# Kernel optimization log

Measured on AMD Instinct MI355X. Metric: run time of the kernel, lower is better.

## Reference

```python
import jax, jax.numpy as jnp
import numpy as np

BS, FH, FW, NA = 32, 100, 100, 9
IMG_H, IMG_W = 1600, 1600
STRIDE = 16
KEEP_PRE, KEEP_POST, NMS_THR = 1000, 300, 0.7


def _grid_anchors():
    scales = np.array([128.0, 256.0, 512.0])
    ratios = np.array([0.5, 1.0, 2.0])
    ws, hs = [], []
    for s in scales:
        for r in ratios:
            ws.append(s * np.sqrt(1.0 / r))
            hs.append(s * np.sqrt(r))
    ws, hs = np.array(ws), np.array(hs)  # [9]
    sx = (np.arange(FW) + 0.5) * STRIDE
    sy = (np.arange(FH) + 0.5) * STRIDE
    cx, cy = np.meshgrid(sx, sy)  # [FH,FW]
    cx = cx.reshape(-1, 1)
    cy = cy.reshape(-1, 1)
    anchors = np.stack([
        cx - 0.5 * ws, cy - 0.5 * hs, cx + 0.5 * ws, cy + 0.5 * hs
    ], axis=-1).reshape(-1, 4)  # [FH*FW*NA, 4]
    return anchors.astype(np.float32)


def setup_inputs() -> dict:
    key = jax.random.key(0)
    k1, k2 = jax.random.split(key)
    N = FH * FW * NA
    cls_logits = jax.random.normal(k1, (BS, N, 1), dtype=jnp.float32)
    reg_deltas = jax.random.normal(k2, (BS, N, 4), dtype=jnp.float32) * 0.3
    anchors = jnp.asarray(_grid_anchors())
    return {"cls_logits": cls_logits, "reg_deltas": reg_deltas,
            "anchors": anchors, "img_h": IMG_H, "img_w": IMG_W}


def _offsets2boxes(deltas, anchors):
    # deltas: [bs,N,4] (dx,dy,dw,dh); anchors: [N,4] xyxy
    aw = anchors[:, 2] - anchors[:, 0]
    ah = anchors[:, 3] - anchors[:, 1]
    acx = anchors[:, 0] + 0.5 * aw
    acy = anchors[:, 1] + 0.5 * ah
    cx = deltas[..., 0] * aw + acx
    cy = deltas[..., 1] * ah + acy
    w = jnp.exp(deltas[..., 2]) * aw
    h = jnp.exp(deltas[..., 3]) * ah
    return jnp.stack([cx - 0.5 * w, cy - 0.5 * h, cx + 0.5 * w, cy + 0.5 * h], axis=-1)


def _iou_matrix(b):
    # b: [K,4] -> [K,K]
    area = (b[:, 2] - b[:, 0]) * (b[:, 3] - b[:, 1])
    lt = jnp.maximum(b[:, None, :2], b[None, :, :2])
    rb = jnp.minimum(b[:, None, 2:], b[None, :, 2:])
    wh = jnp.clip(rb - lt, 0.0)
    inter = wh[..., 0] * wh[..., 1]
    return inter / (area[:, None] + area[None, :] - inter + 1e-12)


def _detect_single(boxes, scores, img_h, img_w):
    # boxes: [N,4], scores: [N]
    top_scores, idx = jax.lax.top_k(scores, KEEP_PRE)
    b = boxes[idx]  # [K,4], already score-sorted descending
    b = jnp.stack([
        jnp.clip(b[:, 0], 0.0, img_w), jnp.clip(b[:, 1], 0.0, img_h),
        jnp.clip(b[:, 2], 0.0, img_w), jnp.clip(b[:, 3], 0.0, img_h)
    ], axis=-1)
    iou = _iou_matrix(b)  # [K,K]
    K = KEEP_PRE
    cols = jnp.arange(K)

    def body(i, keep):
        # if box i still kept, suppress later boxes with IoU > thr (greedy NMS)
        sup = keep[i] & (iou[i] > NMS_THR) & (cols > i)
        return keep & ~sup

    keep = jax.lax.fori_loop(0, K, body, jnp.ones((K,), dtype=bool))
    # kept boxes first (stable sort preserves descending-score order), take top P
    order = jnp.argsort(~keep, stable=True)[:KEEP_POST]
    valid = keep[order]
    det = jnp.concatenate([b[order], top_scores[order, None]], axis=-1)
    return det * valid[:, None].astype(det.dtype)  # padded rows zeroed


def reference(cls_logits, reg_deltas, anchors, img_h, img_w):
    bs = cls_logits.shape[0]
    scores = jax.nn.sigmoid(cls_logits.reshape(bs, -1))  # [bs,N]
    boxes = _offsets2boxes(reg_deltas.reshape(bs, -1, 4), anchors)  # [bs,N,4]
    fh = jnp.float32(img_h)
    fw = jnp.float32(img_w)
    dets = jax.vmap(lambda b, s: _detect_single(b, s, fh, fw))(boxes, scores)
    return dets  # [bs, KEEP_POST, 5] (xmin,ymin,xmax,ymax,score), zero-padded
```

## Files before the change

### kernel.cpp

```cpp
#include <hip/hip_runtime.h>
#include <stdint.h>

#pragma clang fp contract(off)

#define BS 32
#define NANCH 90000
#define KEEP_PRE 1000
#define KEEP_POST 300
#define NMS_THR 0.7f
#define NBINS 4096
#define HREP 4129
#define CAND_MAX 4096
#define MW 16
#define NF4 22500

typedef unsigned long long u64;
typedef unsigned int u32;

#define BOX_OFF    0
#define SCORE_OFF  (BOX_OFF + (size_t)BS * KEEP_PRE * 16)
#define MASK_OFF   (SCORE_OFF + (size_t)BS * KEEP_PRE * 4)

__device__ __forceinline__ u32 fmono(float f) {
    u32 u = __float_as_uint(f);
    return (u & 0x80000000u) ? ~u : (u | 0x80000000u);
}

__global__ __launch_bounds__(1024) void prep_kernel(const float* __restrict__ logits,
                                                    const float* __restrict__ deltas,
                                                    const float* __restrict__ anchors,
                                                    float4* __restrict__ selbox,
                                                    float* __restrict__ selscore,
                                                    const int* __restrict__ p_img_h,
                                                    const int* __restrict__ p_img_w) {
    __shared__ u32 lh[2][HREP];
    __shared__ u32 S[NBINS + 1];
    __shared__ u64 grp[CAND_MAX];
    __shared__ u32 wtot[16], wexc[16];
    __shared__ u32 s_B;
    const int b = blockIdx.x;
    const int tid = threadIdx.x;
    const u32 lane = tid & 63;
    const int wv = tid >> 6;
    u32* h0 = lh[0];
    u32* h1 = lh[1];

    for (int i = tid; i < 2 * HREP; i += 1024) ((u32*)lh)[i] = 0;
    __syncthreads();

    const float4* src4 = (const float4*)(logits + (size_t)b * NANCH);
    u32* myh = lh[tid & 1];

#define H1_(f) do { u32 m_ = fmono(f); atomicAdd(&myh[m_ >> 20], 1u); } while (0)
#define HIST4_(v) do { H1_((v).x); H1_((v).y); H1_((v).z); H1_((v).w); } while (0)

    for (int j = 0; j < 20; j += 4) {
        float4 va = src4[tid + (j + 0) * 1024];
        float4 vb = src4[tid + (j + 1) * 1024];
        float4 vc = src4[tid + (j + 2) * 1024];
        float4 vd = src4[tid + (j + 3) * 1024];
        HIST4_(va); HIST4_(vb); HIST4_(vc); HIST4_(vd);
    }
    {
        float4 ve = src4[tid + 20 * 1024];
        HIST4_(ve);
        if (tid < NF4 - 21 * 1024) {
            float4 vf = src4[tid + 21 * 1024];
            HIST4_(vf);
        }
    }
    __syncthreads();

    const int g = tid * 4;
    const u32 c0 = h0[g] + h1[g];
    const u32 c1 = h0[g + 1] + h1[g + 1];
    const u32 c2 = h0[g + 2] + h1[g + 2];
    const u32 c3 = h0[g + 3] + h1[g + 3];
    {
        u32 s = c0 + c1 + c2 + c3;
#pragma unroll
        for (int off = 1; off < 64; off <<= 1) {
            u32 x = __shfl_down(s, off);
            if (lane + off < 64) s += x;
        }
        if (lane == 0) wtot[wv] = s;
        __syncthreads();
        if (tid < 16) {
            u32 v = wtot[tid];
            u32 t = v;
#pragma unroll
            for (int off = 1; off < 16; off <<= 1) {
                u32 x = __shfl_down(t, off);
                if (tid + off < 16) t += x;
            }
            wexc[tid] = t - v;
        }
        __syncthreads();
        const u32 base = wexc[wv] + s;
        S[g]     = base;
        S[g + 1] = base - c0;
        S[g + 2] = base - c0 - c1;
        S[g + 3] = base - c0 - c1 - c2;
        if (tid == 1023) S[NBINS] = 0;
    }
    __syncthreads();

    {
#pragma unroll
        for (int k = 0; k < 4; k++) {
            int bin = g + k;
            if (S[bin] >= KEEP_PRE && S[bin + 1] < KEEP_PRE) s_B = (u32)bin;
        }
        h0[g] = 0; h0[g + 1] = 0; h0[g + 2] = 0; h0[g + 3] = 0;
    }
    __syncthreads();
    const u32 B = s_B;
    const int n_cap = (int)min(S[B], (u32)CAND_MAX);
    u32* fill = h0;

    for (int j = 0; j < 22; ++j) {
        int idx4 = tid + (j << 10);
        if (idx4 >= NF4) break;
        float4 v = src4[idx4];
        u32 mm[4];
        mm[0] = fmono(v.x); mm[1] = fmono(v.y); mm[2] = fmono(v.z); mm[3] = fmono(v.w);
#pragma unroll
        for (int k = 0; k < 4; k++) {
            u32 bin = mm[k] >> 20;
            if (bin >= B) {
                u32 pos = S[bin + 1] + atomicAdd(&fill[bin], 1u);
                u32 i = (u32)(idx4 * 4 + k);
                if (pos < (u32)CAND_MAX)
                    grp[pos] = ((u64)mm[k] << 32) | (u32)(~i);
            }
        }
    }
    __syncthreads();

    const float W = (float)(*p_img_w);
    const float H = (float)(*p_img_h);
    const float4* d4 = (const float4*)deltas;
    const float4* a4 = (const float4*)anchors;
    for (int p = tid; p < n_cap; p += 1024) {
        const u64 me = grp[p];
        const int bin = (int)(me >> 52);
        const int gb = (int)S[bin + 1];
        const int ge = min((int)S[bin], n_cap);
        int rank = gb;
        int q = gb;
        for (; q + 4 <= ge; q += 4) {
            rank += (grp[q] > me) + (grp[q + 1] > me)
                  + (grp[q + 2] > me) + (grp[q + 3] > me);
        }
        for (; q < ge; q++) rank += (grp[q] > me);
        if (rank < KEEP_PRE) {
            u32 idx = ~(u32)me;
            u32 m = (u32)(me >> 32);
            u32 ub = (m & 0x80000000u) ? (m ^ 0x80000000u) : ~m;
            float logit = __uint_as_float(ub);
            float score = 1.0f / (1.0f + expf(-logit));
            float4 d = d4[(size_t)b * NANCH + idx];
            float4 a = a4[idx];
            float aw = a.z - a.x, ah = a.w - a.y;
            float acx = a.x + 0.5f * aw, acy = a.y + 0.5f * ah;
            float cx = d.x * aw + acx, cy = d.y * ah + acy;
            float w = expf(d.z) * aw, h = expf(d.w) * ah;
            float x1 = cx - 0.5f * w, y1 = cy - 0.5f * h;
            float x2 = cx + 0.5f * w, y2 = cy + 0.5f * h;
            x1 = fminf(fmaxf(x1, 0.0f), W); y1 = fminf(fmaxf(y1, 0.0f), H);
            x2 = fminf(fmaxf(x2, 0.0f), W); y2 = fminf(fmaxf(y2, 0.0f), H);
            selbox[(size_t)b * KEEP_PRE + rank] = make_float4(x1, y1, x2, y2);
            selscore[(size_t)b * KEEP_PRE + rank] = score;
        }
    }
#undef H1_
#undef HIST4_
}

__global__ __launch_bounds__(256) void iou_kernel(const float4* __restrict__ selbox,
                                                  u64* __restrict__ mask) {
    const int b = blockIdx.y;
    const int bx = blockIdx.x;
    int c, w;
    if (bx < 16)      { c = 0; w = bx; }
    else if (bx < 28) { c = 1; w = bx - 12; }
    else if (bx < 36) { c = 2; w = bx - 20; }
    else              { c = 3; w = bx - 24; }
    const int i = c * 256 + threadIdx.x;
    __shared__ float4 cb[64];
    __shared__ float ca[64];
    if (threadIdx.x < 64) {
        int j = w * 64 + threadIdx.x;
        float4 bx4 = (j < KEEP_PRE) ? selbox[(size_t)b * KEEP_PRE + j]
                                    : make_float4(0, 0, 0, 0);
        cb[threadIdx.x] = bx4;
        ca[threadIdx.x] = (bx4.z - bx4.x) * (bx4.w - bx4.y);
    }
    __syncthreads();
    if (i >= KEEP_PRE) return;
    float4 bi = selbox[(size_t)b * KEEP_PRE + i];
    float ai = (bi.z - bi.x) * (bi.w - bi.y);
    const int jbase = w * 64;
    u64 bits = 0;
#pragma unroll 8
    for (int jj = 0; jj < 64; jj++) {
        float4 bj = cb[jj];
        float ltx = fmaxf(bi.x, bj.x), lty = fmaxf(bi.y, bj.y);
        float rbx = fminf(bi.z, bj.z), rby = fminf(bi.w, bj.w);
        float wx = fmaxf(rbx - ltx, 0.0f), wy = fmaxf(rby - lty, 0.0f);
        float inter = wx * wy;
        float denom = ai + ca[jj] - inter + 1e-12f;
        if (inter / denom > NMS_THR) bits |= (1ull << jj);
    }
    int lo = i + 1 - jbase;
    u64 mlo = (lo <= 0) ? ~0ull : ((lo >= 64) ? 0ull : (~0ull << lo));
    int hi = KEEP_PRE - jbase;
    u64 mhi = (hi >= 64) ? ~0ull : ((1ull << hi) - 1ull);
    mask[((size_t)b * KEEP_PRE + i) * MW + w] = bits & mlo & mhi;
}

#define CH_ROWS 64
#define CH_WORDS (CH_ROWS * MW)
#define NCHUNK ((KEEP_PRE + CH_ROWS - 1) / CH_ROWS)

__global__ __launch_bounds__(256) void nms_out_kernel(const u64* __restrict__ mask,
                                                      const float4* __restrict__ selbox,
                                                      const float* __restrict__ selscore,
                                                      float* __restrict__ out) {
    const int b = blockIdx.x;
    __shared__ u64 lbuf[2][CH_WORDS];
    __shared__ u64 keepw[MW];
    __shared__ u32 wpre[MW + 1];
    __shared__ int ls_stop;
    const int tid = threadIdx.x;
    const u64* mrow = mask + (size_t)b * KEEP_PRE * MW;

    auto load_chunk = [&](int c) {
        int idx = tid - 128;
        if (idx < 0) return;
        const int words = (c == NCHUNK - 1)
                            ? (KEEP_PRE - (NCHUNK - 1) * CH_ROWS) * MW
                            : CH_WORDS;
        const u64* gsrc = mrow + (size_t)c * CH_WORDS;
        u64* dst = lbuf[c & 1];
#pragma unroll
        for (int k = 0; k < 4; k++) {
            int off = k * 256 + idx * 2;
            ulonglong2 v;
            if (off < words) v = *(const ulonglong2*)(gsrc + off);
            else { v.x = 0ull; v.y = 0ull; }
            *(ulonglong2*)(dst + off) = v;
        }
    };

    if (tid == 0) ls_stop = 0;
    load_chunk(0);
    __syncthreads();

    u64 remv = 0;
    int kept_total = 0;
    const int lw = tid & 15;
    for (int c = 0; c < NCHUNK; c++) {
        if (c + 1 < NCHUNK) load_chunk(c + 1);
        if (tid < 64) {
            const u64* lb = lbuf[c & 1];
            const int wmin = (c >> 2) << 2;
            const u64 vmask = (lw >= wmin) ? ~0ull : 0ull;
            u64 cur = __shfl(remv, c);
#pragma unroll
            for (int blk = 0; blk < 8; blk++) {
                u64 R[8], rwv[8];
#pragma unroll
                for (int k = 0; k < 8; k++)
                    R[k] = lb[(size_t)(blk * 8 + k) * MW + lw] & vmask;
#pragma unroll
                for (int k = 0; k < 8; k++)
                    rwv[k] = lb[(size_t)(blk * 8 + k) * MW + c];
#pragma unroll
                for (int k = 0; k < 8; k++) {
                    const int p = blk * 8 + k;
                    u64 msk = ((cur >> p) & 1ull) ? 0ull : ~0ull;
                    remv |= R[k] & msk;
                    cur  |= rwv[k] & msk;
                }
            }
            kept_total += 64 - (int)__popcll(cur);
            if (c + 1 < NCHUNK && kept_total >= KEEP_POST) {
                if (lw > c) remv = ~0ull;
                if (tid == 0) ls_stop = 1;
            }
        }
        __syncthreads();
        if (ls_stop) break;
    }

    if (tid < MW) {
        u64 kw = ~remv;
        if (tid == MW - 1) kw &= (1ull << (KEEP_PRE - 64 * (MW - 1))) - 1ull;
        keepw[tid] = kw;
    }
    __syncthreads();
    if (tid == 0) {
        u32 cnt = 0;
        for (int w = 0; w < MW; w++) { wpre[w] = cnt; cnt += (u32)__popcll(keepw[w]); }
        wpre[MW] = cnt;
    }
    __syncthreads();
    const int total = (int)wpre[MW];
    float* outb = out + (size_t)b * KEEP_POST * 5;
    for (int i = tid; i < KEEP_PRE; i += 256) {
        int w = i >> 6;
        u64 kw = keepw[w];
        if ((kw >> (i & 63)) & 1ull) {
            int rank = (int)wpre[w] + __popcll(kw & ((1ull << (i & 63)) - 1ull));
            if (rank < KEEP_POST) {
                float4 bx = selbox[(size_t)b * KEEP_PRE + i];
                float sc = selscore[(size_t)b * KEEP_PRE + i];
                outb[rank * 5 + 0] = bx.x;
                outb[rank * 5 + 1] = bx.y;
                outb[rank * 5 + 2] = bx.z;
                outb[rank * 5 + 3] = bx.w;
                outb[rank * 5 + 4] = sc;
            }
        }
    }
    for (int r = tid; r < KEEP_POST; r += 256) {
        if (r >= total) {
            outb[r * 5 + 0] = 0.0f;
            outb[r * 5 + 1] = 0.0f;
            outb[r * 5 + 2] = 0.0f;
            outb[r * 5 + 3] = 0.0f;
            outb[r * 5 + 4] = 0.0f;
        }
    }
}

extern "C" void kernel_launch(void* const* d_in, const int* in_sizes, int n_in,
                              void* d_out, int out_size, void* d_ws, size_t ws_size,
                              hipStream_t stream) {
    const float* logits  = (const float*)d_in[0];
    const float* deltas  = (const float*)d_in[1];
    const float* anchors = (const float*)d_in[2];
    const int* p_img_h   = (const int*)d_in[3];
    const int* p_img_w   = (const int*)d_in[4];

    char* ws = (char*)d_ws;
    float4* selbox  = (float4*)(ws + BOX_OFF);
    float* selscore = (float*)(ws + SCORE_OFF);
    u64* mask       = (u64*)(ws + MASK_OFF);

    prep_kernel<<<dim3(BS), 1024, 0, stream>>>(logits, deltas, anchors,
                                               selbox, selscore, p_img_h, p_img_w);
    iou_kernel<<<dim3(40, BS), 256, 0, stream>>>(selbox, mask);
    nms_out_kernel<<<BS, 256, 0, stream>>>(mask, selbox, selscore, (float*)d_out);
}
```

Baseline: 170.3 us.

## Split per-image top-k prep into sliced histogram, compaction and rank kernels

The single 32-block prep kernel becomes three kernels. A histogram kernel runs 8 slices per image and writes per-slice histograms to global memory. A compaction kernel rebuilds the prefix sums and scatters candidates using per-slice offsets. A rank kernel computes exact ranks and decodes boxes. The goal is to spread the memory-bound histogram and compaction passes over 256 blocks instead of 32, so more of the GPU's compute units are used. The cost is two extra launches, global-memory round trips for the histograms and candidates, and redundant prefix-sum work in every slice block.

```diff
diff --git a/kernel.cpp b/kernel.cpp
--- a/kernel.cpp
+++ b/kernel.cpp
@@ -10,131 +10,167 @@
 #define NMS_THR 0.7f
 #define NBINS 4096
 #define HREP 4129
+#define NCOPY 4
 #define CAND_MAX 4096
 #define MW 16
 #define NF4 22500
+#define NSL 8
+#define F4_PER_BLK ((NF4 + NSL - 1) / NSL)
 
 typedef unsigned long long u64;
 typedef unsigned int u32;
 
-#define BOX_OFF    0
-#define SCORE_OFF  (BOX_OFF + (size_t)BS * KEEP_PRE * 16)
-#define MASK_OFF   (SCORE_OFF + (size_t)BS * KEEP_PRE * 4)
+#define HISTG_OFF 0
+#define SG_OFF    (HISTG_OFF + (size_t)BS * NSL * NBINS * 4)
+#define GRP_OFF   (SG_OFF + (size_t)BS * NBINS * 4)
+#define BOX_OFF   (GRP_OFF + (size_t)BS * CAND_MAX * 8)
+#define SCORE_OFF (BOX_OFF + (size_t)BS * KEEP_PRE * 16)
+#define MASK_OFF  (SCORE_OFF + (size_t)BS * KEEP_PRE * 4)
 
 __device__ __forceinline__ u32 fmono(float f) {
     u32 u = __float_as_uint(f);
     return (u & 0x80000000u) ? ~u : (u | 0x80000000u);
 }
 
-__global__ __launch_bounds__(1024) void prep_kernel(const float* __restrict__ logits,
-                                                    const float* __restrict__ deltas,
+__global__ __launch_bounds__(1024) void hist8_kernel(const float* __restrict__ logits,
+                                                     u32* __restrict__ histg) {
+    __shared__ u32 lh[NCOPY][HREP];
+    const int b = blockIdx.y, slice = blockIdx.x, tid = threadIdx.x;
+    for (int i = tid; i < NCOPY * HREP; i += 1024) ((u32*)lh)[i] = 0;
+    __syncthreads();
+    const float4* src4 = (const float4*)(logits + (size_t)b * NANCH);
+    const int f0 = slice * F4_PER_BLK;
+    const int f1 = min(f0 + F4_PER_BLK, NF4);
+    u32* myh = lh[tid & (NCOPY - 1)];
+    for (int j = f0 + tid; j < f1; j += 1024) {
+        float4 v = src4[j];
+        atomicAdd(&myh[fmono(v.x) >> 20], 1u);
+        atomicAdd(&myh[fmono(v.y) >> 20], 1u);
+        atomicAdd(&myh[fmono(v.z) >> 20], 1u);
+        atomicAdd(&myh[fmono(v.w) >> 20], 1u);
+    }
+    __syncthreads();
+    u32* dst = histg + ((size_t)b * NSL + slice) * NBINS;
+    for (int i = tid; i < NBINS; i += 1024)
+        dst[i] = lh[0][i] + lh[1][i] + lh[2][i] + lh[3][i];
+}
+
+__global__ __launch_bounds__(1024) void compact8_kernel(const float* __restrict__ logits,
+                                                        const u32* __restrict__ histg,
+                                                        u32* __restrict__ Sg,
+                                                        u64* __restrict__ grp) {
+    __shared__ u32 S[NBINS + 1];
+    __shared__ u32 start[NBINS];
+    __shared__ u32 wtot[16], wexc[16];
+    __shared__ u32 s_B;
+    const int b = blockIdx.y, slice = blockIdx.x, tid = threadIdx.x;
+    const u32 lane = tid & 63;
+    const int wv = tid >> 6;
+    const int g = tid * 4;
+
+    u32 c0 = 0, c1 = 0, c2 = 0, c3 = 0;
+    u32 p0 = 0, p1 = 0, p2 = 0, p3 = 0;
+    const u32* hb = histg + (size_t)b * NSL * NBINS;
+#pragma unroll
+    for (int k = 0; k < NSL; k++) {
+        const uint4 h4 = *(const uint4*)(hb + (size_t)k * NBINS + g);
+        c0 += h4.x; c1 += h4.y; c2 += h4.z; c3 += h4.w;
+        if (k < slice) { p0 += h4.x; p1 += h4.y; p2 += h4.z; p3 += h4.w; }
+    }
+    u32 s = c0 + c1 + c2 + c3;
+#pragma unroll
+    for (int off = 1; off < 64; off <<= 1) {
+        u32 x = __shfl_down(s, off);
+        if (lane + off < 64) s += x;
+    }
+    if (lane == 0) wtot[wv] = s;
+    __syncthreads();
+    if (tid < 16) {
+        u32 v = wtot[tid];
+        u32 t = v;
+#pragma unroll
+        for (int off = 1; off < 16; off <<= 1) {
+            u32 x = __shfl_down(t, off);
+            if (tid + off < 16) t += x;
+        }
+        wexc[tid] = t - v;
+    }
+    __syncthreads();
+    const u32 base = wexc[wv] + s;
+    S[g]     = base;
+    S[g + 1] = base - c0;
+    S[g + 2] = base - c0 - c1;
+    S[g + 3] = base - c0 - c1 - c2;
+    if (tid == 1023) S[NBINS] = 0;
+    __syncthreads();
+
+#pragma unroll
+    for (int k = 0; k < 4; k++) {
+        int bin = g + k;
+        if (S[bin] >= KEEP_PRE && S[bin + 1] < KEEP_PRE) s_B = (u32)bin;
+    }
+    start[g]     = S[g + 1] + p0;
+    start[g + 1] = S[g + 2] + p1;
+    start[g + 2] = S[g + 3] + p2;
+    start[g + 3] = S[g + 4] + p3;
+    __syncthreads();
+    const u32 B = s_B;
+
+    if (slice == 0)
+        *(uint4*)(Sg + (size_t)b * NBINS + g) =
+            make_uint4(S[g], S[g + 1], S[g + 2], S[g + 3]);
+
+    const float4* src4 = (const float4*)(logits + (size_t)b * NANCH);
+    const int f0 = slice * F4_PER_BLK;
+    const int f1 = min(f0 + F4_PER_BLK, NF4);
+    u64* dst = grp + (size_t)b * CAND_MAX;
+    for (int j = f0 + tid; j < f1; j += 1024) {
+        float4 v = src4[j];
+        u32 mm[4];
+        mm[0] = fmono(v.x); mm[1] = fmono(v.y); mm[2] = fmono(v.z); mm[3] = fmono(v.w);
+#pragma unroll
+        for (int k = 0; k < 4; k++) {
+            u32 bin = mm[k] >> 20;
+            if (bin >= B) {
+                u32 pos = atomicAdd(&start[bin], 1u);
+                u32 i = (u32)(j * 4 + k);
+                if (pos < (u32)CAND_MAX)
+                    dst[pos] = ((u64)mm[k] << 32) | (u32)(~i);
+            }
+        }
+    }
+}
+
+__global__ __launch_bounds__(1024) void rank_kernel(const float* __restrict__ deltas,
                                                     const float* __restrict__ anchors,
+                                                    const u32* __restrict__ Sg,
+                                                    const u64* __restrict__ grpg,
                                                     float4* __restrict__ selbox,
                                                     float* __restrict__ selscore,
                                                     const int* __restrict__ p_img_h,
                                                     const int* __restrict__ p_img_w) {
-    __shared__ u32 lh[2][HREP];
     __shared__ u32 S[NBINS + 1];
     __shared__ u64 grp[CAND_MAX];
-    __shared__ u32 wtot[16], wexc[16];
     __shared__ u32 s_B;
-    const int b = blockIdx.x;
-    const int tid = threadIdx.x;
-    const u32 lane = tid & 63;
-    const int wv = tid >> 6;
-    u32* h0 = lh[0];
-    u32* h1 = lh[1];
-
-    for (int i = tid; i < 2 * HREP; i += 1024) ((u32*)lh)[i] = 0;
-    __syncthreads();
-
-    const float4* src4 = (const float4*)(logits + (size_t)b * NANCH);
-    u32* myh = lh[tid & 1];
-
-#define H1_(f) do { u32 m_ = fmono(f); atomicAdd(&myh[m_ >> 20], 1u); } while (0)
-#define HIST4_(v) do { H1_((v).x); H1_((v).y); H1_((v).z); H1_((v).w); } while (0)
-
-    for (int j = 0; j < 20; j += 4) {
-        float4 va = src4[tid + (j + 0) * 1024];
-        float4 vb = src4[tid + (j + 1) * 1024];
-        float4 vc = src4[tid + (j + 2) * 1024];
-        float4 vd = src4[tid + (j + 3) * 1024];
-        HIST4_(va); HIST4_(vb); HIST4_(vc); HIST4_(vd);
-    }
+    const int b = blockIdx.x, tid = threadIdx.x;
+    const int g = tid * 4;
     {
-        float4 ve = src4[tid + 20 * 1024];
-        HIST4_(ve);
-        if (tid < NF4 - 21 * 1024) {
-            float4 vf = src4[tid + 21 * 1024];
-            HIST4_(vf);
-        }
-    }
-    __syncthreads();
-
-    const int g = tid * 4;
-    const u32 c0 = h0[g] + h1[g];
-    const u32 c1 = h0[g + 1] + h1[g + 1];
-    const u32 c2 = h0[g + 2] + h1[g + 2];
-    const u32 c3 = h0[g + 3] + h1[g + 3];
-    {
-        u32 s = c0 + c1 + c2 + c3;
-#pragma unroll
-        for (int off = 1; off < 64; off <<= 1) {
-            u32 x = __shfl_down(s, off);
-            if (lane + off < 64) s += x;
-        }
-        if (lane == 0) wtot[wv] = s;
-        __syncthreads();
-        if (tid < 16) {
-            u32 v = wtot[tid];
-            u32 t = v;
-#pragma unroll
-            for (int off = 1; off < 16; off <<= 1) {
-                u32 x = __shfl_down(t, off);
-                if (tid + off < 16) t += x;
-            }
-            wexc[tid] = t - v;
-        }
-        __syncthreads();
-        const u32 base = wexc[wv] + s;
-        S[g]     = base;
-        S[g + 1] = base - c0;
-        S[g + 2] = base - c0 - c1;
-        S[g + 3] = base - c0 - c1 - c2;
-        if (tid == 1023) S[NBINS] = 0;
-    }
-    __syncthreads();
-
-    {
-#pragma unroll
-        for (int k = 0; k < 4; k++) {
-            int bin = g + k;
-            if (S[bin] >= KEEP_PRE && S[bin + 1] < KEEP_PRE) s_B = (u32)bin;
-        }
-        h0[g] = 0; h0[g + 1] = 0; h0[g + 2] = 0; h0[g + 3] = 0;
+        uint4 v = *(const uint4*)(Sg + (size_t)b * NBINS + g);
+        S[g] = v.x; S[g + 1] = v.y; S[g + 2] = v.z; S[g + 3] = v.w;
+    }
+    if (tid == 1023) S[NBINS] = 0;
+    __syncthreads();
+#pragma unroll
+    for (int k = 0; k < 4; k++) {
+        int bin = g + k;
+        if (S[bin] >= KEEP_PRE && S[bin + 1] < KEEP_PRE) s_B = (u32)bin;
     }
     __syncthreads();
     const u32 B = s_B;
     const int n_cap = (int)min(S[B], (u32)CAND_MAX);
-    u32* fill = h0;
-
-    for (int j = 0; j < 22; ++j) {
-        int idx4 = tid + (j << 10);
-        if (idx4 >= NF4) break;
-        float4 v = src4[idx4];
-        u32 mm[4];
-        mm[0] = fmono(v.x); mm[1] = fmono(v.y); mm[2] = fmono(v.z); mm[3] = fmono(v.w);
-#pragma unroll
-        for (int k = 0; k < 4; k++) {
-            u32 bin = mm[k] >> 20;
-            if (bin >= B) {
-                u32 pos = S[bin + 1] + atomicAdd(&fill[bin], 1u);
-                u32 i = (u32)(idx4 * 4 + k);
-                if (pos < (u32)CAND_MAX)
-                    grp[pos] = ((u64)mm[k] << 32) | (u32)(~i);
-            }
-        }
-    }
+    const u64* src = grpg + (size_t)b * CAND_MAX;
+    for (int i = tid; i < n_cap; i += 1024)
+        grp[i] = src[i];
     __syncthreads();
 
     const float W = (float)(*p_img_w);
@@ -173,8 +209,6 @@
             selscore[(size_t)b * KEEP_PRE + rank] = score;
         }
     }
-#undef H1_
-#undef HIST4_
 }
 
 __global__ __launch_bounds__(256) void iou_kernel(const float4* __restrict__ selbox,
@@ -345,11 +379,16 @@
     const int* p_img_w   = (const int*)d_in[4];
 
     char* ws = (char*)d_ws;
+    u32* histg      = (u32*)(ws + HISTG_OFF);
+    u32* Sg         = (u32*)(ws + SG_OFF);
+    u64* grpg       = (u64*)(ws + GRP_OFF);
     float4* selbox  = (float4*)(ws + BOX_OFF);
     float* selscore = (float*)(ws + SCORE_OFF);
     u64* mask       = (u64*)(ws + MASK_OFF);
 
-    prep_kernel<<<dim3(BS), 1024, 0, stream>>>(logits, deltas, anchors,
+    hist8_kernel<<<dim3(NSL, BS), 1024, 0, stream>>>(logits, histg);
+    compact8_kernel<<<dim3(NSL, BS), 1024, 0, stream>>>(logits, histg, Sg, grpg);
+    rank_kernel<<<dim3(BS), 1024, 0, stream>>>(deltas, anchors, Sg, grpg,
                                                selbox, selscore, p_img_h, p_img_w);
     iou_kernel<<<dim3(40, BS), 256, 0, stream>>>(selbox, mask);
     nms_out_kernel<<<BS, 256, 0, stream>>>(mask, selbox, selscore, (float*)d_out);
```

New measurement: 159.2 us (median of 2 runs). 6.5% less time.

## Split top-k selection into per-slice candidate kernel plus merge kernel

Applied to the files above, without the earlier changes.

Top-k selection no longer runs as one 1024-thread block per batch item. Each batch item is now split across 8 slices, so 256 blocks do histogram and threshold filtering over about 11k logits each. Each slice keeps its local candidates (local top ~1000 superset) in global workspace, compacted with wave ballots. A second per-batch kernel re-histograms the merged candidates, picks the threshold bin, scatters into shared memory and ranks them. The goal is to fix the low occupancy of 32 blocks reading 90k logits twice. The cost is an extra launch, a global round-trip of candidates, and capacity caps that could drop candidates in skewed inputs.

```diff
diff --git a/kernel.cpp b/kernel.cpp
--- a/kernel.cpp
+++ b/kernel.cpp
@@ -10,128 +10,197 @@
 #define NMS_THR 0.7f
 #define NBINS 4096
 #define HREP 4129
-#define CAND_MAX 4096
 #define MW 16
 #define NF4 22500
+#define NSL 8
+#define F4_PER_BLK ((NF4 + NSL - 1) / NSL)
+#define SLICE_CAP 1536
+#define MERGE_CAP 2048
 
 typedef unsigned long long u64;
 typedef unsigned int u32;
 
-#define BOX_OFF    0
-#define SCORE_OFF  (BOX_OFF + (size_t)BS * KEEP_PRE * 16)
-#define MASK_OFF   (SCORE_OFF + (size_t)BS * KEEP_PRE * 4)
+#define CNTG_OFF  0
+#define CAND_OFF  1024
+#define BOX_OFF   (CAND_OFF + (size_t)BS * NSL * SLICE_CAP * 8)
+#define SCORE_OFF (BOX_OFF + (size_t)BS * KEEP_PRE * 16)
+#define MASK_OFF  (SCORE_OFF + (size_t)BS * KEEP_PRE * 4)
 
 __device__ __forceinline__ u32 fmono(float f) {
     u32 u = __float_as_uint(f);
     return (u & 0x80000000u) ? ~u : (u | 0x80000000u);
 }
 
-__global__ __launch_bounds__(1024) void prep_kernel(const float* __restrict__ logits,
-                                                    const float* __restrict__ deltas,
-                                                    const float* __restrict__ anchors,
-                                                    float4* __restrict__ selbox,
-                                                    float* __restrict__ selscore,
-                                                    const int* __restrict__ p_img_h,
-                                                    const int* __restrict__ p_img_w) {
+__global__ __launch_bounds__(1024) void sel_kernel(const float* __restrict__ logits,
+                                                   u32* __restrict__ cntg,
+                                                   u64* __restrict__ cand) {
+    __shared__ u32 mono[F4_PER_BLK * 4 + 12];
     __shared__ u32 lh[2][HREP];
+    __shared__ u32 wtot[16], wexc[16];
+    __shared__ u32 s_B, s_cnt;
+    const int b = blockIdx.y, slice = blockIdx.x, tid = threadIdx.x;
+    const u32 lane = tid & 63;
+    const int wv = tid >> 6;
+
+    for (int i = tid; i < 2 * HREP; i += 1024) ((u32*)lh)[i] = 0;
+    if (tid == 0) s_cnt = 0;
+    __syncthreads();
+
+    const float4* src4 = (const float4*)(logits + (size_t)b * NANCH);
+    const int f0 = slice * F4_PER_BLK;
+    const int f1 = min(f0 + F4_PER_BLK, NF4);
+    const int nf = f1 - f0;
+    u32* myh = lh[tid & 1];
+    for (int j = tid; j < nf; j += 1024) {
+        float4 v = src4[f0 + j];
+        u32 m0 = fmono(v.x), m1 = fmono(v.y), m2 = fmono(v.z), m3 = fmono(v.w);
+        *(uint4*)&mono[j * 4] = make_uint4(m0, m1, m2, m3);
+        atomicAdd(&myh[m0 >> 20], 1u);
+        atomicAdd(&myh[m1 >> 20], 1u);
+        atomicAdd(&myh[m2 >> 20], 1u);
+        atomicAdd(&myh[m3 >> 20], 1u);
+    }
+    __syncthreads();
+
+    const int g = tid * 4;
+    const u32 c0 = lh[0][g] + lh[1][g];
+    const u32 c1 = lh[0][g + 1] + lh[1][g + 1];
+    const u32 c2 = lh[0][g + 2] + lh[1][g + 2];
+    const u32 c3 = lh[0][g + 3] + lh[1][g + 3];
+    u32 sc = c0 + c1 + c2 + c3;
+#pragma unroll
+    for (int off = 1; off < 64; off <<= 1) {
+        u32 x = __shfl_down(sc, off);
+        if (lane + off < 64) sc += x;
+    }
+    if (lane == 0) wtot[wv] = sc;
+    __syncthreads();
+    if (tid < 16) {
+        u32 v = wtot[tid];
+        u32 t = v;
+#pragma unroll
+        for (int off = 1; off < 16; off <<= 1) {
+            u32 x = __shfl_down(t, off);
+            if (tid + off < 16) t += x;
+        }
+        wexc[tid] = t - v;
+    }
+    __syncthreads();
+    {
+        const u32 S0 = wexc[wv] + sc;
+        const u32 S1 = S0 - c0, S2 = S1 - c1, S3 = S2 - c2, S4 = S3 - c3;
+        if (S0 >= KEEP_PRE && S1 < KEEP_PRE) s_B = (u32)g;
+        if (S1 >= KEEP_PRE && S2 < KEEP_PRE) s_B = (u32)(g + 1);
+        if (S2 >= KEEP_PRE && S3 < KEEP_PRE) s_B = (u32)(g + 2);
+        if (S3 >= KEEP_PRE && S4 < KEEP_PRE) s_B = (u32)(g + 3);
+    }
+    __syncthreads();
+    const u32 B = s_B;
+
+    const int ntot = nf * 4;
+    const int npad = ((ntot + 1023) & ~1023);
+    u64* dst = cand + ((size_t)b * NSL + slice) * SLICE_CAP;
+    for (int i = tid; i < npad; i += 1024) {
+        u32 m = (i < ntot) ? mono[i] : 0u;
+        bool is = (i < ntot) && ((m >> 20) >= B);
+        u64 bal = __ballot(is);
+        if (bal) {
+            u32 old = 0;
+            if (lane == 0) old = atomicAdd(&s_cnt, (u32)__popcll(bal));
+            u32 wbase = __shfl(old, 0);
+            if (is) {
+                u32 prefix = (u32)__popcll(bal & ((1ull << lane) - 1ull));
+                u32 pos = wbase + prefix;
+                if (pos < SLICE_CAP) {
+                    u32 gi = (u32)(f0 * 4 + i);
+                    dst[pos] = ((u64)m << 32) | (u32)(~gi);
+                }
+            }
+        }
+    }
+    __syncthreads();
+    if (tid == 0) cntg[b * NSL + slice] = min(s_cnt, (u32)SLICE_CAP);
+}
+
+__global__ __launch_bounds__(1024) void merge_kernel(const float* __restrict__ deltas,
+                                                     const float* __restrict__ anchors,
+                                                     const u32* __restrict__ cntg,
+                                                     const u64* __restrict__ cand,
+                                                     float4* __restrict__ selbox,
+                                                     float* __restrict__ selscore,
+                                                     const int* __restrict__ p_img_h,
+                                                     const int* __restrict__ p_img_w) {
+    __shared__ u32 lh[HREP];
     __shared__ u32 S[NBINS + 1];
-    __shared__ u64 grp[CAND_MAX];
+    __shared__ u32 start[NBINS];
+    __shared__ u64 grp[MERGE_CAP];
     __shared__ u32 wtot[16], wexc[16];
     __shared__ u32 s_B;
-    const int b = blockIdx.x;
-    const int tid = threadIdx.x;
+    const int b = blockIdx.x, tid = threadIdx.x;
     const u32 lane = tid & 63;
     const int wv = tid >> 6;
-    u32* h0 = lh[0];
-    u32* h1 = lh[1];
-
-    for (int i = tid; i < 2 * HREP; i += 1024) ((u32*)lh)[i] = 0;
-    __syncthreads();
-
-    const float4* src4 = (const float4*)(logits + (size_t)b * NANCH);
-    u32* myh = lh[tid & 1];
-
-#define H1_(f) do { u32 m_ = fmono(f); atomicAdd(&myh[m_ >> 20], 1u); } while (0)
-#define HIST4_(v) do { H1_((v).x); H1_((v).y); H1_((v).z); H1_((v).w); } while (0)
-
-    for (int j = 0; j < 20; j += 4) {
-        float4 va = src4[tid + (j + 0) * 1024];
-        float4 vb = src4[tid + (j + 1) * 1024];
-        float4 vc = src4[tid + (j + 2) * 1024];
-        float4 vd = src4[tid + (j + 3) * 1024];
-        HIST4_(va); HIST4_(vb); HIST4_(vc); HIST4_(vd);
-    }
+
+    for (int i = tid; i < HREP; i += 1024) lh[i] = 0;
+    __syncthreads();
+
+    u32 cnts[NSL];
+#pragma unroll
+    for (int k = 0; k < NSL; k++) cnts[k] = cntg[b * NSL + k];
+    const u64* src = cand + (size_t)b * NSL * SLICE_CAP;
+
+#pragma unroll
+    for (int k = 0; k < NSL; k++) {
+        const u64* ss = src + (size_t)k * SLICE_CAP;
+        for (int i = tid; i < (int)cnts[k]; i += 1024)
+            atomicAdd(&lh[(u32)(ss[i] >> 52)], 1u);
+    }
+    __syncthreads();
+
+    const int g = tid * 4;
+    const u32 c0 = lh[g], c1 = lh[g + 1], c2 = lh[g + 2], c3 = lh[g + 3];
+    u32 sc = c0 + c1 + c2 + c3;
+#pragma unroll
+    for (int off = 1; off < 64; off <<= 1) {
+        u32 x = __shfl_down(sc, off);
+        if (lane + off < 64) sc += x;
+    }
+    if (lane == 0) wtot[wv] = sc;
+    __syncthreads();
+    if (tid < 16) {
+        u32 v = wtot[tid];
+        u32 t = v;
+#pragma unroll
+        for (int off = 1; off < 16; off <<= 1) {
+            u32 x = __shfl_down(t, off);
+            if (tid + off < 16) t += x;
+        }
+        wexc[tid] = t - v;
+    }
+    __syncthreads();
     {
-        float4 ve = src4[tid + 20 * 1024];
-        HIST4_(ve);
-        if (tid < NF4 - 21 * 1024) {
-            float4 vf = src4[tid + 21 * 1024];
-            HIST4_(vf);
-        }
-    }
-    __syncthreads();
-
-    const int g = tid * 4;
-    const u32 c0 = h0[g] + h1[g];
-    const u32 c1 = h0[g + 1] + h1[g + 1];
-    const u32 c2 = h0[g + 2] + h1[g + 2];
-    const u32 c3 = h0[g + 3] + h1[g + 3];
-    {
-        u32 s = c0 + c1 + c2 + c3;
-#pragma unroll
-        for (int off = 1; off < 64; off <<= 1) {
-            u32 x = __shfl_down(s, off);
-            if (lane + off < 64) s += x;
-        }
-        if (lane == 0) wtot[wv] = s;
-        __syncthreads();
-        if (tid < 16) {
-            u32 v = wtot[tid];
-            u32 t = v;
-#pragma unroll
-            for (int off = 1; off < 16; off <<= 1) {
-                u32 x = __shfl_down(t, off);
-                if (tid + off < 16) t += x;
-            }
-            wexc[tid] = t - v;
-        }
-        __syncthreads();
-        const u32 base = wexc[wv] + s;
-        S[g]     = base;
-        S[g + 1] = base - c0;
-        S[g + 2] = base - c0 - c1;
-        S[g + 3] = base - c0 - c1 - c2;
+        const u32 S0 = wexc[wv] + sc;
+        const u32 S1 = S0 - c0, S2 = S1 - c1, S3 = S2 - c2, S4 = S3 - c3;
+        S[g] = S0; S[g + 1] = S1; S[g + 2] = S2; S[g + 3] = S3;
         if (tid == 1023) S[NBINS] = 0;
-    }
-    __syncthreads();
-
-    {
-#pragma unroll
-        for (int k = 0; k < 4; k++) {
-            int bin = g + k;
-            if (S[bin] >= KEEP_PRE && S[bin + 1] < KEEP_PRE) s_B = (u32)bin;
-        }
-        h0[g] = 0; h0[g + 1] = 0; h0[g + 2] = 0; h0[g + 3] = 0;
+        start[g] = S1; start[g + 1] = S2; start[g + 2] = S3; start[g + 3] = S4;
+        if (S0 >= KEEP_PRE && S1 < KEEP_PRE) s_B = (u32)g;
+        if (S1 >= KEEP_PRE && S2 < KEEP_PRE) s_B = (u32)(g + 1);
+        if (S2 >= KEEP_PRE && S3 < KEEP_PRE) s_B = (u32)(g + 2);
+        if (S3 >= KEEP_PRE && S4 < KEEP_PRE) s_B = (u32)(g + 3);
     }
     __syncthreads();
     const u32 B = s_B;
-    const int n_cap = (int)min(S[B], (u32)CAND_MAX);
-    u32* fill = h0;
-
-    for (int j = 0; j < 22; ++j) {
-        int idx4 = tid + (j << 10);
-        if (idx4 >= NF4) break;
-        float4 v = src4[idx4];
-        u32 mm[4];
-        mm[0] = fmono(v.x); mm[1] = fmono(v.y); mm[2] = fmono(v.z); mm[3] = fmono(v.w);
-#pragma unroll
-        for (int k = 0; k < 4; k++) {
-            u32 bin = mm[k] >> 20;
+    const int n_cap = (int)min(S[B], (u32)MERGE_CAP);
+
+#pragma unroll
+    for (int k = 0; k < NSL; k++) {
+        const u64* ss = src + (size_t)k * SLICE_CAP;
+        for (int i = tid; i < (int)cnts[k]; i += 1024) {
+            u64 key = ss[i];
+            u32 bin = (u32)(key >> 52);
             if (bin >= B) {
-                u32 pos = S[bin + 1] + atomicAdd(&fill[bin], 1u);
-                u32 i = (u32)(idx4 * 4 + k);
-                if (pos < (u32)CAND_MAX)
-                    grp[pos] = ((u64)mm[k] << 32) | (u32)(~i);
+                u32 pos = atomicAdd(&start[bin], 1u);
+                if (pos < (u32)MERGE_CAP) grp[pos] = key;
             }
         }
     }
@@ -173,8 +242,6 @@
             selscore[(size_t)b * KEEP_PRE + rank] = score;
         }
     }
-#undef H1_
-#undef HIST4_
 }
 
 __global__ __launch_bounds__(256) void iou_kernel(const float4* __restrict__ selbox,
@@ -345,12 +412,15 @@
     const int* p_img_w   = (const int*)d_in[4];
 
     char* ws = (char*)d_ws;
+    u32* cntg       = (u32*)(ws + CNTG_OFF);
+    u64* cand       = (u64*)(ws + CAND_OFF);
     float4* selbox  = (float4*)(ws + BOX_OFF);
     float* selscore = (float*)(ws + SCORE_OFF);
     u64* mask       = (u64*)(ws + MASK_OFF);
 
-    prep_kernel<<<dim3(BS), 1024, 0, stream>>>(logits, deltas, anchors,
-                                               selbox, selscore, p_img_h, p_img_w);
+    sel_kernel<<<dim3(NSL, BS), 1024, 0, stream>>>(logits, cntg, cand);
+    merge_kernel<<<dim3(BS), 1024, 0, stream>>>(deltas, anchors, cntg, cand,
+                                                selbox, selscore, p_img_h, p_img_w);
     iou_kernel<<<dim3(40, BS), 256, 0, stream>>>(selbox, mask);
     nms_out_kernel<<<BS, 256, 0, stream>>>(mask, selbox, selscore, (float*)d_out);
 }
```

Result: faster. 160.9 us (-5.5%).
